# Optimization experiments

Measured on AMD Instinct MI355X. Metric: run time of the kernel, lower is better.

Reference implementation:

```python
import jax, jax.numpy as jnp
import numpy as np

IN_F = 8192
OUT_F = 8192
R = 16
LORA_ALPHA = 32
BLOCK = 64
SCALING = LORA_ALPHA / R  # 2.0
NUMEL = IN_F * OUT_F


def dequantize_4bit(packed, scales):
    # packed: [numel//2] bytes (stored as int32 in [0,255]); element 2i = low nibble, 2i+1 = high nibble
    low = packed & 0xF
    high = (packed >> 4) & 0xF
    q = jnp.stack([low, high], axis=-1).reshape(-1)          # [numel] ints in [0,15]
    flat = q.astype(jnp.float32) - 8.0                        # signed 4-bit
    flat = (flat.reshape(-1, BLOCK) * scales[:, None]).reshape(-1)  # blockwise scale
    return flat.reshape(OUT_F, IN_F)


def setup_inputs() -> dict:
    key = jax.random.key(0)
    k1, k2, k3, k4, k5 = jax.random.split(key, 5)
    x = jax.random.normal(k1, (1, 64, IN_F), dtype=jnp.float32)
    packed_weights = jax.random.randint(k2, (NUMEL // 2,), 0, 256, dtype=jnp.int32)
    block_scales = jax.random.uniform(k3, (NUMEL // BLOCK,), dtype=jnp.float32) * 0.05
    # kaiming_uniform(a=sqrt(5)) on [R, IN_F] -> bound = 1/sqrt(IN_F)
    bound = 1.0 / np.sqrt(IN_F)
    lora_A = jax.random.uniform(k4, (R, IN_F), minval=-bound, maxval=bound, dtype=jnp.float32)
    # original init is zeros; use small randn for a non-trivial baseline
    lora_B = jax.random.normal(k5, (OUT_F, R), dtype=jnp.float32) * 0.02
    return {"x": x, "packed_weights": packed_weights, "block_scales": block_scales,
            "lora_A": lora_A, "lora_B": lora_B}


def reference(x, packed_weights, block_scales, lora_A, lora_B):
    W = dequantize_4bit(packed_weights, block_scales).astype(x.dtype)  # [OUT_F, IN_F]
    base_out = jnp.einsum('bsi,oi->bso', x, W)                         # no bias (bias_buffer=None)
    lora_out = jnp.einsum('bsr,or->bso', jnp.einsum('bsi,ri->bsr', x, lora_A), lora_B) * SCALING
    return base_out + lora_out
```

## Files before the change

kernel.cpp:

```cpp
#include <hip/hip_runtime.h>
#include <hip/hip_bf16.h>

#define IN_F 8192
#define OUT_F 8192
#define SEQ 64
#define LORA_R 16

typedef __attribute__((ext_vector_type(4))) float f32x4;
typedef __attribute__((ext_vector_type(4))) int i32x4;
typedef __attribute__((ext_vector_type(8))) unsigned short u16x8;
typedef __attribute__((ext_vector_type(4))) unsigned short u16x4;
typedef _Float16 f16x2 __attribute__((ext_vector_type(2)));
typedef _Float16 f16x8 __attribute__((ext_vector_type(8)));

typedef __attribute__((address_space(3))) unsigned int lds_u32;
typedef const __attribute__((address_space(1))) unsigned int glb_u32;

__device__ __forceinline__ void gl_lds16(const void* g, void* l) {
    __builtin_amdgcn_global_load_lds((glb_u32*)g, (lds_u32*)l, 16, 0, 0);
}

__global__ __launch_bounds__(256) void k_prep(
    const float* __restrict__ x, const float* __restrict__ A,
    unsigned short* __restrict__ xb, float* __restrict__ t) {
    __shared__ float part[64];
    const int s = blockIdx.x >> 2, p = blockIdx.x & 3;
    const int w = threadIdx.x >> 6, lane = threadIdx.x & 63;
    const int kbase = p * 2048 + w * 512;
    const float* xr = x + s * IN_F + kbase;

    f32x4 xv[2];
    #pragma unroll
    for (int j = 0; j < 2; ++j) {
        xv[j] = *(const f32x4*)(xr + j * 256 + lane * 4);
        u16x4 h;
        h[0] = __builtin_bit_cast(unsigned short, (_Float16)xv[j].x);
        h[1] = __builtin_bit_cast(unsigned short, (_Float16)xv[j].y);
        h[2] = __builtin_bit_cast(unsigned short, (_Float16)xv[j].z);
        h[3] = __builtin_bit_cast(unsigned short, (_Float16)xv[j].w);
        *(u16x4*)(xb + s * IN_F + kbase + j * 256 + lane * 4) = h;
    }

    float acc[LORA_R];
    #pragma unroll
    for (int r = 0; r < LORA_R; ++r) acc[r] = 0.f;
    #pragma unroll
    for (int r = 0; r < LORA_R; ++r) {
        const float* ar = A + r * IN_F + kbase;
        #pragma unroll
        for (int j = 0; j < 2; ++j) {
            f32x4 av = *(const f32x4*)(ar + j * 256 + lane * 4);
            acc[r] = fmaf(xv[j].x, av.x, acc[r]);
            acc[r] = fmaf(xv[j].y, av.y, acc[r]);
            acc[r] = fmaf(xv[j].z, av.z, acc[r]);
            acc[r] = fmaf(xv[j].w, av.w, acc[r]);
        }
    }
    #pragma unroll
    for (int r = 0; r < LORA_R; ++r) {
        float v = acc[r];
        #pragma unroll
        for (int off = 32; off; off >>= 1) v += __shfl_down(v, off, 64);
        if (lane == 0) part[w * 16 + r] = v;
    }
    __syncthreads();
    if (threadIdx.x < 16)
        t[s * 64 + p * 16 + threadIdx.x] = part[threadIdx.x] + part[16 + threadIdx.x] +
                                           part[32 + threadIdx.x] + part[48 + threadIdx.x];
}

__global__ __launch_bounds__(512, 2) void k_main(
    const int* __restrict__ packed, const float* __restrict__ scales,
    const unsigned short* __restrict__ xb, const float* __restrict__ t,
    const float* __restrict__ B, float* __restrict__ out) {
    __shared__ char lds[115200];
    _Float16* xs = (_Float16*)lds;
    int* wt = (int*)(lds + 65536);
    float* scs = (float*)(lds + 98304);
    float* accs = (float*)lds;
    float* tred = scs;

    const int tid = threadIdx.x;
    const int n0 = blockIdx.x * 32;
    const int w = tid >> 6, lane = tid & 63;
    const int nh = w >> 2, wkk = w & 3;
    const int q = lane >> 4, c16 = lane & 15;

    const int lrow = lane >> 4, lcol = lane & 15;
    const int xr0 = w * 8 + lrow, xr1 = xr0 + 4;
    const int wr  = w * 4 + lrow;
    const unsigned short* xg0 = xb + (size_t)xr0 * IN_F + ((lcol ^ (xr0 & 7)) << 3);
    const unsigned short* xg1 = xb + (size_t)xr1 * IN_F + ((lcol ^ (xr1 & 7)) << 3);
    const int* wgp = packed + (long)(n0 + wr) * (IN_F / 2) + ((lcol ^ (wr & 7)) << 2);

    _Float16* xd0 = xs + w * 8 * 128;
    _Float16* xd1 = xd0 + 4 * 128;
    int* wd = wt + w * 256;

    {
        int row = tid >> 4, g = tid & 15;
        const float* sp = scales + (n0 + row) * (IN_F / 64);
        *(f32x4*)(scs + row * 132 + g * 4)      = *(const f32x4*)(sp + g * 4);
        *(f32x4*)(scs + row * 132 + 64 + g * 4) = *(const f32x4*)(sp + 64 + g * 4);
    }

    f32x4 acc[4];
    #pragma unroll
    for (int mt = 0; mt < 4; ++mt) acc[mt] = (f32x4){0.f, 0.f, 0.f, 0.f};

    const int pvo = (nh * 16 + c16) * 64 + ((wkk * 16 + q * 4) ^ ((c16 & 7) << 2));
    int afo[4];
    #pragma unroll
    for (int mt = 0; mt < 4; ++mt)
        afo[mt] = (mt * 16 + c16) * 128 + ((wkk * 32 + q * 8) ^ ((c16 & 7) << 3));
    const int sco = (nh * 16 + c16) * 132 + (wkk >> 1);

    asm volatile("s_waitcnt lgkmcnt(0)" ::: "memory");
    __builtin_amdgcn_s_barrier();

    #pragma unroll
    for (int c = 0; c < 3; ++c) {
        gl_lds16(xg0 + (size_t)c * 128, xd0 + c * 8192);
        gl_lds16(xg1 + (size_t)c * 128, xd1 + c * 8192);
        gl_lds16(wgp + c * 64,          wd  + c * 2048);
    }

    const f16x2 c1032 = {(_Float16)1032.0f, (_Float16)1032.0f};

    for (int kt = 0; kt < 64; ++kt) {
        if (kt < 62)       asm volatile("s_waitcnt vmcnt(6)" ::: "memory");
        else if (kt == 62) asm volatile("s_waitcnt vmcnt(3)" ::: "memory");
        else               asm volatile("s_waitcnt vmcnt(0)" ::: "memory");
        __builtin_amdgcn_s_barrier();
        __builtin_amdgcn_sched_barrier(0);
        const int cur = kt & 3;
        if (kt < 61) {
            const int nxt = (kt + 3) & 3;
            const size_t xoff = (size_t)(kt + 3) * 128;
            gl_lds16(xg0 + xoff, xd0 + nxt * 8192);
            gl_lds16(xg1 + xoff, xd1 + nxt * 8192);
            gl_lds16(wgp + (kt + 3) * 64, wd + nxt * 2048);
        }
        i32x4 pv = *(const i32x4*)(wt + cur * 2048 + pvo);
        float scf = scs[sco + kt * 2];
        _Float16 sch = (_Float16)scf;
        f16x2 sc2 = {sch, sch};
        f16x8 bf;
        #pragma unroll
        for (int m = 0; m < 4; ++m) {
            unsigned u = ((((unsigned)pv[m] << 12) | (unsigned)pv[m]) & 0x000F000Fu) | 0x64006400u;
            f16x2 h = __builtin_bit_cast(f16x2, u);
            h = (h - c1032) * sc2;
            bf[2 * m] = h.x;
            bf[2 * m + 1] = h.y;
        }
        const _Float16* xbase = xs + cur * 8192;
        #pragma unroll
        for (int mt = 0; mt < 4; ++mt) {
            f16x8 af = *(const f16x8*)(xbase + afo[mt]);
            acc[mt] = __builtin_amdgcn_mfma_f32_16x16x32_f16(af, bf, acc[mt], 0, 0, 0);
        }
    }
    __syncthreads();

    float* myacc = accs + w * (64 * 17);
    #pragma unroll
    for (int mt = 0; mt < 4; ++mt)
        #pragma unroll
        for (int r = 0; r < 4; ++r)
            myacc[(mt * 16 + q * 4 + r) * 17 + c16] = acc[mt][r];
    #pragma unroll
    for (int jj = 0; jj < 2; ++jj) {
        int p2 = tid + jj * 512;
        const float* tp = t + (p2 >> 4) * 64 + (p2 & 15);
        tred[p2] = tp[0] + tp[16] + tp[32] + tp[48];
    }
    __syncthreads();

    #pragma unroll
    for (int j = 0; j < 4; ++j) {
        int p = tid + j * 512;
        int s = p >> 5, c = p & 31;
        const float* ab = accs + (c >> 4) * 4 * (64 * 17) + s * 17 + (c & 15);
        float v = ab[0] + ab[64 * 17] + ab[2 * 64 * 17] + ab[3 * 64 * 17];
        const float* trow = tred + s * 16;
        const float* bp = B + (n0 + c) * LORA_R;
        f32x4 t0 = *(const f32x4*)trow,        t1 = *(const f32x4*)(trow + 4);
        f32x4 t2 = *(const f32x4*)(trow + 8),  t3 = *(const f32x4*)(trow + 12);
        f32x4 b0 = *(const f32x4*)bp,       b1 = *(const f32x4*)(bp + 4);
        f32x4 b2 = *(const f32x4*)(bp + 8), b3 = *(const f32x4*)(bp + 12);
        float lr = t0.x * b0.x + t0.y * b0.y + t0.z * b0.z + t0.w * b0.w
                 + t1.x * b1.x + t1.y * b1.y + t1.z * b1.z + t1.w * b1.w
                 + t2.x * b2.x + t2.y * b2.y + t2.z * b2.z + t2.w * b2.w
                 + t3.x * b3.x + t3.y * b3.y + t3.z * b3.z + t3.w * b3.w;
        v += 2.0f * lr;
        out[s * OUT_F + n0 + c] = v;
    }
}

extern "C" void kernel_launch(void* const* d_in, const int* in_sizes, int n_in,
                              void* d_out, int out_size, void* d_ws, size_t ws_size,
                              hipStream_t stream) {
    const float* x      = (const float*)d_in[0];
    const int* packed   = (const int*)d_in[1];
    const float* scales = (const float*)d_in[2];
    const float* lora_A = (const float*)d_in[3];
    const float* lora_B = (const float*)d_in[4];
    float* out = (float*)d_out;

    unsigned short* xb = (unsigned short*)d_ws;
    float* t = (float*)((char*)d_ws + (size_t)SEQ * IN_F * 2);

    k_prep<<<256, 256, 0, stream>>>(x, lora_A, xb, t);
    k_main<<<256, 512, 0, stream>>>(packed, scales, xb, t, lora_B, out);
}
```

Before: 217.1 us.

## Replace LDS-staged pipeline with direct register loads and smaller column tiles

Drops the async global-to-LDS multi-buffered pipeline in the main GEMV kernel. Each wave now loads packed weights and fp16 activations directly into registers, double-buffered in software, and splits K across all 8 waves. Column tiles shrink from 32 to 16, doubling the grid to 512 blocks, and the LDS footprint drops so occupancy can rise to 4 blocks per CU. Scales are stored in LDS as fp16 and the LoRA B rows are staged in LDS. The risk is that activations are reread from global or L2 by every block without LDS sharing, and register double-buffering may hide latency less well than the deep async pipeline.

```diff
diff --git a/kernel.cpp b/kernel.cpp
--- a/kernel.cpp
+++ b/kernel.cpp
@@ -8,17 +8,9 @@
 
 typedef __attribute__((ext_vector_type(4))) float f32x4;
 typedef __attribute__((ext_vector_type(4))) int i32x4;
-typedef __attribute__((ext_vector_type(8))) unsigned short u16x8;
 typedef __attribute__((ext_vector_type(4))) unsigned short u16x4;
 typedef _Float16 f16x2 __attribute__((ext_vector_type(2)));
 typedef _Float16 f16x8 __attribute__((ext_vector_type(8)));
-
-typedef __attribute__((address_space(3))) unsigned int lds_u32;
-typedef const __attribute__((address_space(1))) unsigned int glb_u32;
-
-__device__ __forceinline__ void gl_lds16(const void* g, void* l) {
-    __builtin_amdgcn_global_load_lds((glb_u32*)g, (lds_u32*)l, 16, 0, 0);
-}
 
 __global__ __launch_bounds__(256) void k_prep(
     const float* __restrict__ x, const float* __restrict__ A,
@@ -69,98 +61,106 @@
                                            part[32 + threadIdx.x] + part[48 + threadIdx.x];
 }
 
-__global__ __launch_bounds__(512, 2) void k_main(
+__global__ __launch_bounds__(512, 4) void k_main(
     const int* __restrict__ packed, const float* __restrict__ scales,
     const unsigned short* __restrict__ xb, const float* __restrict__ t,
     const float* __restrict__ B, float* __restrict__ out) {
-    __shared__ char lds[115200];
-    _Float16* xs = (_Float16*)lds;
-    int* wt = (int*)(lds + 65536);
-    float* scs = (float*)(lds + 98304);
+    __shared__ char lds[40000];
+    _Float16* scs = (_Float16*)lds;
     float* accs = (float*)lds;
-    float* tred = scs;
+    float* tred = (float*)(lds + 34816);
+    float* bs   = (float*)(lds + 38912);
 
     const int tid = threadIdx.x;
-    const int n0 = blockIdx.x * 32;
+    const int n0 = blockIdx.x * 16;
     const int w = tid >> 6, lane = tid & 63;
-    const int nh = w >> 2, wkk = w & 3;
     const int q = lane >> 4, c16 = lane & 15;
 
-    const int lrow = lane >> 4, lcol = lane & 15;
-    const int xr0 = w * 8 + lrow, xr1 = xr0 + 4;
-    const int wr  = w * 4 + lrow;
-    const unsigned short* xg0 = xb + (size_t)xr0 * IN_F + ((lcol ^ (xr0 & 7)) << 3);
-    const unsigned short* xg1 = xb + (size_t)xr1 * IN_F + ((lcol ^ (xr1 & 7)) << 3);
-    const int* wgp = packed + (long)(n0 + wr) * (IN_F / 2) + ((lcol ^ (wr & 7)) << 2);
-
-    _Float16* xd0 = xs + w * 8 * 128;
-    _Float16* xd1 = xd0 + 4 * 128;
-    int* wd = wt + w * 256;
-
-    {
+    if (tid < 256) {
         int row = tid >> 4, g = tid & 15;
-        const float* sp = scales + (n0 + row) * (IN_F / 64);
-        *(f32x4*)(scs + row * 132 + g * 4)      = *(const f32x4*)(sp + g * 4);
-        *(f32x4*)(scs + row * 132 + 64 + g * 4) = *(const f32x4*)(sp + 64 + g * 4);
-    }
+        const float* sp = scales + (size_t)(n0 + row) * (IN_F / 64) + g * 8;
+        f32x4 a = *(const f32x4*)sp;
+        f32x4 b = *(const f32x4*)(sp + 4);
+        u16x4 ha, hb;
+        ha[0] = __builtin_bit_cast(unsigned short, (_Float16)a.x);
+        ha[1] = __builtin_bit_cast(unsigned short, (_Float16)a.y);
+        ha[2] = __builtin_bit_cast(unsigned short, (_Float16)a.z);
+        ha[3] = __builtin_bit_cast(unsigned short, (_Float16)a.w);
+        hb[0] = __builtin_bit_cast(unsigned short, (_Float16)b.x);
+        hb[1] = __builtin_bit_cast(unsigned short, (_Float16)b.y);
+        hb[2] = __builtin_bit_cast(unsigned short, (_Float16)b.z);
+        hb[3] = __builtin_bit_cast(unsigned short, (_Float16)b.w);
+        *(u16x4*)((unsigned short*)scs + row * 132 + g * 8)     = ha;
+        *(u16x4*)((unsigned short*)scs + row * 132 + g * 8 + 4) = hb;
+    }
+    __syncthreads();
+
+    const int* wp = packed + (size_t)(n0 + c16) * (IN_F / 2) + w * 16 + q * 4;
+    const _Float16* xf0 = (const _Float16*)xb + (size_t)(c16)      * IN_F + w * 32 + q * 8;
+    const _Float16* xf1 = (const _Float16*)xb + (size_t)(16 + c16) * IN_F + w * 32 + q * 8;
+    const _Float16* xf2 = (const _Float16*)xb + (size_t)(32 + c16) * IN_F + w * 32 + q * 8;
+    const _Float16* xf3 = (const _Float16*)xb + (size_t)(48 + c16) * IN_F + w * 32 + q * 8;
+    const int sci = c16 * 132 + (w >> 1);
 
     f32x4 acc[4];
     #pragma unroll
     for (int mt = 0; mt < 4; ++mt) acc[mt] = (f32x4){0.f, 0.f, 0.f, 0.f};
 
-    const int pvo = (nh * 16 + c16) * 64 + ((wkk * 16 + q * 4) ^ ((c16 & 7) << 2));
-    int afo[4];
-    #pragma unroll
-    for (int mt = 0; mt < 4; ++mt)
-        afo[mt] = (mt * 16 + c16) * 128 + ((wkk * 32 + q * 8) ^ ((c16 & 7) << 3));
-    const int sco = (nh * 16 + c16) * 132 + (wkk >> 1);
-
-    asm volatile("s_waitcnt lgkmcnt(0)" ::: "memory");
-    __builtin_amdgcn_s_barrier();
-
-    #pragma unroll
-    for (int c = 0; c < 3; ++c) {
-        gl_lds16(xg0 + (size_t)c * 128, xd0 + c * 8192);
-        gl_lds16(xg1 + (size_t)c * 128, xd1 + c * 8192);
-        gl_lds16(wgp + c * 64,          wd  + c * 2048);
-    }
-
     const f16x2 c1032 = {(_Float16)1032.0f, (_Float16)1032.0f};
 
-    for (int kt = 0; kt < 64; ++kt) {
-        if (kt < 62)       asm volatile("s_waitcnt vmcnt(6)" ::: "memory");
-        else if (kt == 62) asm volatile("s_waitcnt vmcnt(3)" ::: "memory");
-        else               asm volatile("s_waitcnt vmcnt(0)" ::: "memory");
-        __builtin_amdgcn_s_barrier();
-        __builtin_amdgcn_sched_barrier(0);
-        const int cur = kt & 3;
-        if (kt < 61) {
-            const int nxt = (kt + 3) & 3;
-            const size_t xoff = (size_t)(kt + 3) * 128;
-            gl_lds16(xg0 + xoff, xd0 + nxt * 8192);
-            gl_lds16(xg1 + xoff, xd1 + nxt * 8192);
-            gl_lds16(wgp + (kt + 3) * 64, wd + nxt * 2048);
-        }
-        i32x4 pv = *(const i32x4*)(wt + cur * 2048 + pvo);
-        float scf = scs[sco + kt * 2];
-        _Float16 sch = (_Float16)scf;
-        f16x2 sc2 = {sch, sch};
-        f16x8 bf;
-        #pragma unroll
-        for (int m = 0; m < 4; ++m) {
-            unsigned u = ((((unsigned)pv[m] << 12) | (unsigned)pv[m]) & 0x000F000Fu) | 0x64006400u;
-            f16x2 h = __builtin_bit_cast(f16x2, u);
-            h = (h - c1032) * sc2;
-            bf[2 * m] = h.x;
-            bf[2 * m + 1] = h.y;
-        }
-        const _Float16* xbase = xs + cur * 8192;
-        #pragma unroll
-        for (int mt = 0; mt < 4; ++mt) {
-            f16x8 af = *(const f16x8*)(xbase + afo[mt]);
-            acc[mt] = __builtin_amdgcn_mfma_f32_16x16x32_f16(af, bf, acc[mt], 0, 0, 0);
-        }
-    }
+    i32x4 pvA, pvB;
+    f16x8 afA0, afA1, afA2, afA3, afB0, afB1, afB2, afB3;
+    pvA = *(const i32x4*)wp;
+    afA0 = *(const f16x8*)xf0; afA1 = *(const f16x8*)xf1;
+    afA2 = *(const f16x8*)xf2; afA3 = *(const f16x8*)xf3;
+
+    for (int kt = 0; kt < 32; kt += 2) {
+        if (kt + 1 < 32) {
+            const size_t wo = (size_t)(kt + 1) * 128, xo = (size_t)(kt + 1) * 256;
+            pvB = *(const i32x4*)(wp + wo);
+            afB0 = *(const f16x8*)(xf0 + xo); afB1 = *(const f16x8*)(xf1 + xo);
+            afB2 = *(const f16x8*)(xf2 + xo); afB3 = *(const f16x8*)(xf3 + xo);
+        }
+        {
+            _Float16 sch = scs[sci + kt * 4];
+            f16x2 sc2 = {sch, sch};
+            f16x8 bf;
+            #pragma unroll
+            for (int m = 0; m < 4; ++m) {
+                unsigned u = ((((unsigned)pvA[m] << 12) | (unsigned)pvA[m]) & 0x000F000Fu) | 0x64006400u;
+                f16x2 h = __builtin_bit_cast(f16x2, u);
+                h = (h - c1032) * sc2;
+                bf[2 * m] = h.x; bf[2 * m + 1] = h.y;
+            }
+            acc[0] = __builtin_amdgcn_mfma_f32_16x16x32_f16(afA0, bf, acc[0], 0, 0, 0);
+            acc[1] = __builtin_amdgcn_mfma_f32_16x16x32_f16(afA1, bf, acc[1], 0, 0, 0);
+            acc[2] = __builtin_amdgcn_mfma_f32_16x16x32_f16(afA2, bf, acc[2], 0, 0, 0);
+            acc[3] = __builtin_amdgcn_mfma_f32_16x16x32_f16(afA3, bf, acc[3], 0, 0, 0);
+        }
+        if (kt + 2 < 32) {
+            const size_t wo = (size_t)(kt + 2) * 128, xo = (size_t)(kt + 2) * 256;
+            pvA = *(const i32x4*)(wp + wo);
+            afA0 = *(const f16x8*)(xf0 + xo); afA1 = *(const f16x8*)(xf1 + xo);
+            afA2 = *(const f16x8*)(xf2 + xo); afA3 = *(const f16x8*)(xf3 + xo);
+        }
+        if (kt + 1 < 32) {
+            _Float16 sch = scs[sci + (kt + 1) * 4];
+            f16x2 sc2 = {sch, sch};
+            f16x8 bf;
+            #pragma unroll
+            for (int m = 0; m < 4; ++m) {
+                unsigned u = ((((unsigned)pvB[m] << 12) | (unsigned)pvB[m]) & 0x000F000Fu) | 0x64006400u;
+                f16x2 h = __builtin_bit_cast(f16x2, u);
+                h = (h - c1032) * sc2;
+                bf[2 * m] = h.x; bf[2 * m + 1] = h.y;
+            }
+            acc[0] = __builtin_amdgcn_mfma_f32_16x16x32_f16(afB0, bf, acc[0], 0, 0, 0);
+            acc[1] = __builtin_amdgcn_mfma_f32_16x16x32_f16(afB1, bf, acc[1], 0, 0, 0);
+            acc[2] = __builtin_amdgcn_mfma_f32_16x16x32_f16(afB2, bf, acc[2], 0, 0, 0);
+            acc[3] = __builtin_amdgcn_mfma_f32_16x16x32_f16(afB3, bf, acc[3], 0, 0, 0);
+        }
+    }
+
     __syncthreads();
 
     float* myacc = accs + w * (64 * 17);
@@ -175,26 +175,26 @@
         const float* tp = t + (p2 >> 4) * 64 + (p2 & 15);
         tred[p2] = tp[0] + tp[16] + tp[32] + tp[48];
     }
-    __syncthreads();
-
-    #pragma unroll
-    for (int j = 0; j < 4; ++j) {
+    if (tid < 256) {
+        int row = tid >> 4, r = tid & 15;
+        bs[row * 17 + r] = B[(size_t)(n0 + row) * LORA_R + r];
+    }
+    __syncthreads();
+
+    #pragma unroll
+    for (int j = 0; j < 2; ++j) {
         int p = tid + j * 512;
-        int s = p >> 5, c = p & 31;
-        const float* ab = accs + (c >> 4) * 4 * (64 * 17) + s * 17 + (c & 15);
-        float v = ab[0] + ab[64 * 17] + ab[2 * 64 * 17] + ab[3 * 64 * 17];
+        int s = p >> 4, c = p & 15;
+        const float* ap = accs + s * 17 + c;
+        float v = 0.f;
+        #pragma unroll
+        for (int ww = 0; ww < 8; ++ww) v += ap[ww * (64 * 17)];
         const float* trow = tred + s * 16;
-        const float* bp = B + (n0 + c) * LORA_R;
-        f32x4 t0 = *(const f32x4*)trow,        t1 = *(const f32x4*)(trow + 4);
-        f32x4 t2 = *(const f32x4*)(trow + 8),  t3 = *(const f32x4*)(trow + 12);
-        f32x4 b0 = *(const f32x4*)bp,       b1 = *(const f32x4*)(bp + 4);
-        f32x4 b2 = *(const f32x4*)(bp + 8), b3 = *(const f32x4*)(bp + 12);
-        float lr = t0.x * b0.x + t0.y * b0.y + t0.z * b0.z + t0.w * b0.w
-                 + t1.x * b1.x + t1.y * b1.y + t1.z * b1.z + t1.w * b1.w
-                 + t2.x * b2.x + t2.y * b2.y + t2.z * b2.z + t2.w * b2.w
-                 + t3.x * b3.x + t3.y * b3.y + t3.z * b3.z + t3.w * b3.w;
-        v += 2.0f * lr;
-        out[s * OUT_F + n0 + c] = v;
+        const float* brow = bs + c * 17;
+        float lr = 0.f;
+        #pragma unroll
+        for (int r = 0; r < 16; ++r) lr = fmaf(trow[r], brow[r], lr);
+        out[(size_t)s * OUT_F + n0 + c] = v + 2.0f * lr;
     }
 }
 
@@ -212,5 +212,5 @@
     float* t = (float*)((char*)d_ws + (size_t)SEQ * IN_F * 2);
 
     k_prep<<<256, 256, 0, stream>>>(x, lora_A, xb, t);
-    k_main<<<256, 512, 0, stream>>>(packed, scales, xb, t, lora_B, out);
+    k_main<<<512, 512, 0, stream>>>(packed, scales, xb, t, lora_B, out);
 }
```

Result: slower. 257.1 us (+18.4%).
